# Performance work log

Hardware: AMD Instinct MI355X
Metric: run time of the kernel (lower is better)

## Reference

```python
import jax, jax.numpy as jnp
import numpy as np

B, L, D, E, N, DDELTA, DCONV = 4, 2048, 1024, 2048, 16, 64, 4
EPS = 1e-5


def setup_inputs() -> dict:
    key = jax.random.key(0)
    ks = jax.random.split(key, 12)
    def rn(k, shape, scale=0.02):
        return (jax.random.normal(k, shape) * scale).astype(jnp.float32)
    return {
        "resid":  jax.random.normal(ks[0], (B, L, D), dtype=jnp.float32),
        "norm_w": jnp.ones((D,), jnp.float32),
        "skip_w": rn(ks[1], (E, D)),          # skip_proj.weight
        "in_w":   rn(ks[2], (E, D)),          # in_proj.weight
        "conv_w": rn(ks[3], (E, 1, DCONV), 0.1),  # depthwise conv1d weight
        "conv_b": jnp.zeros((E,), jnp.float32),
        "Wd1":    rn(ks[4], (DDELTA, E)),     # W_delta_1.weight
        "Wd2_w":  rn(ks[5], (E, DDELTA)),     # W_delta_2.weight
        "Wd2_b":  rn(ks[6], (E,), 0.01),      # W_delta_2.bias
        "WB":     rn(ks[7], (N, E)),          # W_B.weight
        "WC":     rn(ks[8], (N, E)),          # W_C.weight
        "A_log":  (jax.random.normal(ks[9], (E, N)) * 0.5).astype(jnp.float32),
        "W_D":    jnp.ones((E,), jnp.float32),
        "out_w":  rn(ks[10], (D, E)),         # out_proj.weight
    }


def reference(resid, norm_w, skip_w, in_w, conv_w, conv_b, Wd1, Wd2_w, Wd2_b,
              WB, WC, A_log, W_D, out_w):
    # RMSNorm
    x = resid * jax.lax.rsqrt(jnp.mean(resid * resid, axis=-1, keepdims=True) + EPS) * norm_w
    skip = x @ skip_w.T                              # [B,L,E]
    x = x @ in_w.T                                   # [B,L,E]
    # depthwise causal conv1d (padding=DCONV-1 then truncate to L == left-pad only)
    xc = jnp.transpose(x, (0, 2, 1))                 # [B,E,L]
    xc = jax.lax.conv_general_dilated(
        xc, conv_w, window_strides=(1,), padding=[(DCONV - 1, 0)],
        dimension_numbers=("NCH", "OIH", "NCH"), feature_group_count=conv_w.shape[0])
    x = jnp.transpose(xc, (0, 2, 1)) + conv_b        # [B,L,E]
    x = jax.nn.silu(x)                               # ssm input

    A = -jnp.exp(A_log)                              # [E,N]
    delta = jax.nn.softplus((x @ Wd1.T) @ Wd2_w.T + Wd2_b)  # [B,L,E]
    Bm = x @ WB.T                                    # [B,L,N]
    Cm = x @ WC.T                                    # [B,L,N]

    def step(h, inp):
        x_l, d_l, B_l, C_l = inp                     # [B,E],[B,E],[B,N],[B,N]
        A_bar = jnp.exp(d_l[:, :, None] * A)         # [B,E,N]
        h = A_bar * h + (d_l * x_l)[:, :, None] * B_l[:, None, :]
        y_l = jnp.einsum("ben,bn->be", h, C_l)       # h @ C
        return h, y_l

    h0 = jnp.zeros((resid.shape[0], A.shape[0], A.shape[1]), x.dtype)
    xs = (jnp.swapaxes(x, 0, 1), jnp.swapaxes(delta, 0, 1),
          jnp.swapaxes(Bm, 0, 1), jnp.swapaxes(Cm, 0, 1))
    _, ys = jax.lax.scan(step, h0, xs)               # ys: [L,B,E]
    y = jnp.swapaxes(ys, 0, 1)                       # [B,L,E]

    y = y + x * W_D
    y = y * jax.nn.silu(skip)
    y = y @ out_w.T                                  # [B,L,D]
    return resid + y
```

## Files before the change

### kernel.cpp

```cpp
#include <hip/hip_runtime.h>
#include <hip/hip_bf16.h>
#include <math.h>

#define B_ 4
#define L_ 2048
#define D_ 1024
#define E_ 2048
#define N_ 16
#define DD_ 64
#define DCONV_ 4

#define S_SEG 32
#define SEGLEN_ (L_ / S_SEG)

typedef __attribute__((ext_vector_type(8))) short bf16x8;
typedef __attribute__((ext_vector_type(4))) float f32x4;

typedef __attribute__((address_space(1))) const void gvoid_t;
typedef __attribute__((address_space(3))) void lvoid_t;

static __device__ __forceinline__ float silu_f(float x) {
    return x / (1.f + __expf(-x));
}

static __device__ __forceinline__ ushort f2bf(float f) {
    __hip_bfloat16 h = __float2bfloat16(f);
    return *reinterpret_cast<ushort*>(&h);
}

static __device__ __forceinline__ float bf2f(ushort u) {
    uint v = ((uint)u) << 16;
    return __uint_as_float(v);
}

#define LOG2E_ 1.4426950408889634f

__global__ __launch_bounds__(256) void k_rmsnorm_bf(const float* __restrict__ resid,
                                                    const float* __restrict__ nw,
                                                    ushort* __restrict__ out) {
    int row = blockIdx.x;
    const float* r = resid + (size_t)row * D_;
    int t = threadIdx.x;
    float4 v = *reinterpret_cast<const float4*>(&r[t * 4]);
    float ss = v.x * v.x + v.y * v.y + v.z * v.z + v.w * v.w;
#pragma unroll
    for (int o = 32; o >= 1; o >>= 1) ss += __shfl_xor(ss, o, 64);
    __shared__ float red[4];
    if ((t & 63) == 0) red[t >> 6] = ss;
    __syncthreads();
    float tot = red[0] + red[1] + red[2] + red[3];
    float rs = rsqrtf(tot * (1.f / (float)D_) + 1e-5f);
    float4 w4 = *reinterpret_cast<const float4*>(&nw[t * 4]);
    ushort4 o4;
    o4.x = f2bf(v.x * rs * w4.x);
    o4.y = f2bf(v.y * rs * w4.y);
    o4.z = f2bf(v.z * rs * w4.z);
    o4.w = f2bf(v.w * rs * w4.w);
    *reinterpret_cast<ushort4*>(&out[(size_t)row * D_ + t * 4]) = o4;
}

__global__ __launch_bounds__(256) void k_cast_all(const float* __restrict__ skip_w,
                                                  const float* __restrict__ in_w,
                                                  const float* __restrict__ out_w,
                                                  const float* __restrict__ WB,
                                                  const float* __restrict__ WC,
                                                  const float* __restrict__ Wd1,
                                                  const float* __restrict__ Wd2,
                                                  ushort* __restrict__ w2,
                                                  ushort* __restrict__ outw,
                                                  ushort* __restrict__ wbc,
                                                  ushort* __restrict__ wd2) {
    int i = blockIdx.x * 256 + threadIdx.x;
    const float* src;
    ushort* dst;
    int off;
    if (i < 524288)       { src = skip_w; dst = w2;            off = i; }
    else if (i < 1048576) { src = in_w;   dst = w2 + 2097152;  off = i - 524288; }
    else if (i < 1572864) { src = out_w;  dst = outw;          off = i - 1048576; }
    else if (i < 1581056) { src = WB;     dst = wbc;           off = i - 1572864; }
    else if (i < 1589248) { src = WC;     dst = wbc + 32768;   off = i - 1581056; }
    else if (i < 1622016) { src = Wd1;    dst = wbc + 65536;   off = i - 1589248; }
    else                  { src = Wd2;    dst = wd2;           off = i - 1622016; }
    float4 v = *reinterpret_cast<const float4*>(&src[(size_t)off * 4]);
    ushort4 o;
    o.x = f2bf(v.x); o.y = f2bf(v.y); o.z = f2bf(v.z); o.w = f2bf(v.w);
    *reinterpret_cast<ushort4*>(&dst[(size_t)off * 4]) = o;
}

template <int EPI>
__global__ __launch_bounds__(256) void k_gemm_bf(const ushort* __restrict__ A,
                                                 const ushort* __restrict__ W,
                                                 const float* __restrict__ bias,
                                                 const float* __restrict__ addsrc,
                                                 float* __restrict__ Cf,
                                                 ushort* __restrict__ Cbf,
                                                 ushort* __restrict__ Cbf2,
                                                 int M, int N, int K) {
    constexpr int BM = 128, BN = 128, BK = 32;
    union SM {
        ushort stage[2 * BM * BK];
        float  epi[4][16][65];
    };
    __shared__ __align__(16) SM sm;
    ushort* As = sm.stage;
    ushort* Ws = sm.stage + BM * BK;

    int t = threadIdx.x;
    int m0 = blockIdx.y * BM, n0 = blockIdx.x * BN;
    int wave = t >> 6, lane = t & 63;
    int wr = wave >> 1, wc = wave & 1;
    int lr = lane & 15, lg = lane >> 4;
    int srow = lane >> 2;
    int scol = (lane & 3) * 8;

    f32x4 acc[4][4] = {};

    for (int k0 = 0; k0 < K; k0 += BK) {
#pragma unroll
        for (int p = 0; p < 2; ++p) {
            int seg = wave * 2 + p;
            int row = seg * 16 + srow;
            __builtin_amdgcn_global_load_lds(
                (gvoid_t*)(A + (size_t)(m0 + row) * K + k0 + scol),
                (lvoid_t*)(As + seg * 512), 16, 0, 0);
            __builtin_amdgcn_global_load_lds(
                (gvoid_t*)(W + (size_t)(n0 + row) * K + k0 + scol),
                (lvoid_t*)(Ws + seg * 512), 16, 0, 0);
        }
        __syncthreads();
        bf16x8 af[4], bfr[4];
#pragma unroll
        for (int i = 0; i < 4; ++i) {
            af[i]  = *reinterpret_cast<const bf16x8*>(&As[(wr * 64 + i * 16 + lr) * BK + lg * 8]);
            bfr[i] = *reinterpret_cast<const bf16x8*>(&Ws[(wc * 64 + i * 16 + lr) * BK + lg * 8]);
        }
#pragma unroll
        for (int i = 0; i < 4; ++i)
#pragma unroll
            for (int j = 0; j < 4; ++j)
                acc[i][j] = __builtin_amdgcn_mfma_f32_16x16x32_bf16(af[i], bfr[j], acc[i][j], 0, 0, 0);
        __syncthreads();
    }

    int er = lane >> 2;
    int ec = (lane & 3) * 16;
#pragma unroll
    for (int i = 0; i < 4; ++i) {
#pragma unroll
        for (int j = 0; j < 4; ++j)
#pragma unroll
            for (int q = 0; q < 4; ++q)
                sm.epi[wave][lg * 4 + q][j * 16 + lr] = acc[i][j][q];
        float vals[16];
#pragma unroll
        for (int v4 = 0; v4 < 4; ++v4) {
            f32x4 tmp = *reinterpret_cast<const f32x4*>(&sm.epi[wave][er][ec + v4 * 4]);
            vals[v4 * 4 + 0] = tmp[0]; vals[v4 * 4 + 1] = tmp[1];
            vals[v4 * 4 + 2] = tmp[2]; vals[v4 * 4 + 3] = tmp[3];
        }
        int grow = m0 + wr * 64 + i * 16 + er;
        int gcol = n0 + wc * 64 + ec;

        if (EPI == 1) {
            ushort u[16];
#pragma unroll
            for (int k = 0; k < 16; ++k) {
                float z = vals[k] + bias[gcol + k];
                u[k] = f2bf((z > 20.f) ? z : log1pf(expf(z)));
            }
            *reinterpret_cast<uint4*>(&Cbf[(size_t)grow * N + gcol]) = *reinterpret_cast<uint4*>(&u[0]);
            *reinterpret_cast<uint4*>(&Cbf[(size_t)grow * N + gcol + 8]) = *reinterpret_cast<uint4*>(&u[8]);
        } else if (EPI == 2) {
#pragma unroll
            for (int v4 = 0; v4 < 4; ++v4) {
                f32x4 r4 = *reinterpret_cast<const f32x4*>(&addsrc[(size_t)grow * N + gcol + v4 * 4]);
                f32x4 o4;
#pragma unroll
                for (int k = 0; k < 4; ++k) o4[k] = vals[v4 * 4 + k] + r4[k];
                *reinterpret_cast<f32x4*>(&Cf[(size_t)grow * N + gcol + v4 * 4]) = o4;
            }
        } else {
            ushort u[16];
#pragma unroll
            for (int k = 0; k < 16; ++k) u[k] = f2bf(vals[k]);
            if (gcol < 2048) {
                *reinterpret_cast<uint4*>(&Cbf[(size_t)grow * 2048 + gcol]) = *reinterpret_cast<uint4*>(&u[0]);
                *reinterpret_cast<uint4*>(&Cbf[(size_t)grow * 2048 + gcol + 8]) = *reinterpret_cast<uint4*>(&u[8]);
            } else {
                int c2 = gcol - 2048;
                *reinterpret_cast<uint4*>(&Cbf2[(size_t)grow * 2048 + c2]) = *reinterpret_cast<uint4*>(&u[0]);
                *reinterpret_cast<uint4*>(&Cbf2[(size_t)grow * 2048 + c2 + 8]) = *reinterpret_cast<uint4*>(&u[8]);
            }
        }
    }
}

__global__ __launch_bounds__(256) void k_proj(const ushort* __restrict__ A,
                                              const ushort* __restrict__ Wc,
                                              float* __restrict__ Bm,
                                              float* __restrict__ Cm,
                                              ushort* __restrict__ d1_bf) {
    constexpr int BK = 32, LDB = 40;
    __shared__ __align__(16) ushort As[32 * LDB];
    __shared__ __align__(16) ushort Ws[96 * LDB];
    int t = threadIdx.x;
    int m0 = blockIdx.x * 32;
    int wave = t >> 6, lane = t & 63;
    int rowbase = (wave >> 1) * 16;
    int colbase = (wave & 1) * 48;
    int lr = lane & 15, lg = lane >> 4;

    f32x4 acc[3] = {};

    for (int k0 = 0; k0 < E_; k0 += BK) {
        if (t < 128) {
            int row = t >> 2;
            int cg = (t & 3) * 8;
            *reinterpret_cast<uint4*>(&As[row * LDB + cg]) =
                *reinterpret_cast<const uint4*>(&A[(size_t)(m0 + row) * E_ + k0 + cg]);
        }
        {
            int row = t >> 2, cg = (t & 3) * 8;
            *reinterpret_cast<uint4*>(&Ws[row * LDB + cg]) =
                *reinterpret_cast<const uint4*>(&Wc[(size_t)row * E_ + k0 + cg]);
            if (t < 128) {
                int f2 = t + 256;
                int row2 = f2 >> 2, cg2 = (f2 & 3) * 8;
                *reinterpret_cast<uint4*>(&Ws[row2 * LDB + cg2]) =
                    *reinterpret_cast<const uint4*>(&Wc[(size_t)row2 * E_ + k0 + cg2]);
            }
        }
        __syncthreads();
        bf16x8 af = *reinterpret_cast<const bf16x8*>(&As[(rowbase + lr) * LDB + lg * 8]);
#pragma unroll
        for (int j = 0; j < 3; ++j) {
            bf16x8 bf = *reinterpret_cast<const bf16x8*>(&Ws[(colbase + j * 16 + lr) * LDB + lg * 8]);
            acc[j] = __builtin_amdgcn_mfma_f32_16x16x32_bf16(af, bf, acc[j], 0, 0, 0);
        }
        __syncthreads();
    }

#pragma unroll
    for (int j = 0; j < 3; ++j) {
        int ncol = colbase + j * 16 + lr;
#pragma unroll
        for (int q = 0; q < 4; ++q) {
            int m = m0 + rowbase + lg * 4 + q;
            float v = acc[j][q];
            if (ncol < 16)      Bm[(size_t)m * 16 + ncol] = v;
            else if (ncol < 32) Cm[(size_t)m * 16 + (ncol - 16)] = v;
            else                d1_bf[(size_t)m * 64 + (ncol - 32)] = f2bf(v);
        }
    }
}

__global__ __launch_bounds__(256) void k_conv_silu(const ushort* __restrict__ x,
                                                   const float* __restrict__ w,
                                                   const float* __restrict__ bias,
                                                   ushort* __restrict__ out_bf) {
    int idx = blockIdx.x * 256 + threadIdx.x;
    int e = idx & (E_ - 1);
    int l = (idx / E_) & (L_ - 1);
    float4 wv = *reinterpret_cast<const float4*>(&w[e * 4]);
    float acc = bias[e];
    acc = fmaf(wv.w, bf2f(x[idx]), acc);
    if (l >= 1) acc = fmaf(wv.z, bf2f(x[idx - E_]), acc);
    if (l >= 2) acc = fmaf(wv.y, bf2f(x[idx - 2 * E_]), acc);
    if (l >= 3) acc = fmaf(wv.x, bf2f(x[idx - 3 * E_]), acc);
    out_bf[idx] = f2bf(silu_f(acc));
}

__global__ __launch_bounds__(256, 4) void k_scan_p1(const ushort* __restrict__ xs,
                                                    const ushort* __restrict__ delta,
                                                    const float* __restrict__ Bm,
                                                    const float* __restrict__ A_log,
                                                    float* __restrict__ hbuf,
                                                    float* __restrict__ sdsum) {
    int t = threadIdx.x;
    int bid = blockIdx.x;
    int s = bid & (S_SEG - 1);
    int eblk = (bid >> 5) & 7;
    int b = bid >> 8;
    int e = eblk * 256 + t;

    float A2[16];
#pragma unroll
    for (int i = 0; i < 16; i += 4) {
        f32x4 al = *reinterpret_cast<const f32x4*>(&A_log[(size_t)e * 16 + i]);
#pragma unroll
        for (int j = 0; j < 4; ++j) A2[i + j] = -__expf(al[j]) * LOG2E_;
    }
    f32x4 h4[4] = {};
    float sdl = 0.f;

    const ushort* dp = delta + ((size_t)b * L_ + s * SEGLEN_) * E_ + e;
    const ushort* xp = xs    + ((size_t)b * L_ + s * SEGLEN_) * E_ + e;
    const float*  Bp = Bm + ((size_t)b * L_ + s * SEGLEN_) * 16;

    auto compute = [&](ushort du, ushort xu, int l) {
        float d = bf2f(du), xv = bf2f(xu);
        float dx = d * xv;
        sdl += d;
#pragma unroll
        for (int g = 0; g < 4; ++g) {
            f32x4 Bv = *reinterpret_cast<const f32x4*>(&Bp[l * 16 + g * 4]);
            f32x4 e4;
#pragma unroll
            for (int j = 0; j < 4; ++j) e4[j] = exp2f(d * A2[g * 4 + j]);
            h4[g] = e4 * h4[g] + dx * Bv;
        }
    };

    ushort duA = dp[0], xuA = xp[0];
    for (int l = 0; l < SEGLEN_; l += 2) {
        ushort duB = dp[(l + 1) * E_], xuB = xp[(l + 1) * E_];
        compute(duA, xuA, l);
        int ln = l + 2; if (ln > SEGLEN_ - 1) ln = SEGLEN_ - 1;
        duA = dp[ln * E_]; xuA = xp[ln * E_];
        compute(duB, xuB, l + 1);
    }

    size_t cidx = ((size_t)(b * S_SEG + s) * E_ + e) * 16;
#pragma unroll
    for (int g = 0; g < 4; ++g)
        *reinterpret_cast<f32x4*>(&hbuf[cidx + g * 4]) = h4[g];
    sdsum[(size_t)(b * S_SEG + s) * E_ + e] = sdl;
}

__global__ __launch_bounds__(256) void k_scan_p2(float* __restrict__ hbuf,
                                                 const float* __restrict__ sdsum,
                                                 const float* __restrict__ A_log) {
    int t = blockIdx.x * 256 + threadIdx.x;
    int q = t & 3;
    int e = (t >> 2) & (E_ - 1);
    int b = t >> 13;
    f32x4 A2;
    {
        f32x4 al = *reinterpret_cast<const f32x4*>(&A_log[(size_t)e * 16 + q * 4]);
#pragma unroll
        for (int i = 0; i < 4; ++i) A2[i] = -__expf(al[i]) * LOG2E_;
    }
    f32x4 acc = {0.f, 0.f, 0.f, 0.f};
    for (int s = 0; s < S_SEG; ++s) {
        size_t idx = ((size_t)(b * S_SEG + s) * E_ + e) * 16 + q * 4;
        f32x4 hl = *reinterpret_cast<const f32x4*>(&hbuf[idx]);
        float sd = sdsum[(size_t)(b * S_SEG + s) * E_ + e];
        *reinterpret_cast<f32x4*>(&hbuf[idx]) = acc;
        f32x4 p;
#pragma unroll
        for (int i = 0; i < 4; ++i) p[i] = exp2f(A2[i] * sd);
        acc = hl + p * acc;
    }
}

__global__ __launch_bounds__(256, 4) void k_scan_p3(const ushort* __restrict__ xs,
                                                    const ushort* __restrict__ delta,
                                                    const float* __restrict__ Bm,
                                                    const float* __restrict__ Cm,
                                                    const float* __restrict__ A_log,
                                                    const float* __restrict__ W_D,
                                                    const ushort* __restrict__ skip,
                                                    const float* __restrict__ hbuf,
                                                    ushort* __restrict__ yg) {
    int t = threadIdx.x;
    int bid = blockIdx.x;
    int s = bid & (S_SEG - 1);
    int eblk = (bid >> 5) & 7;
    int b = bid >> 8;
    int e = eblk * 256 + t;

    float A2[16];
#pragma unroll
    for (int i = 0; i < 16; i += 4) {
        f32x4 al = *reinterpret_cast<const f32x4*>(&A_log[(size_t)e * 16 + i]);
#pragma unroll
        for (int j = 0; j < 4; ++j) A2[i + j] = -__expf(al[j]) * LOG2E_;
    }
    size_t cidx = ((size_t)(b * S_SEG + s) * E_ + e) * 16;
    f32x4 h4[4];
#pragma unroll
    for (int g = 0; g < 4; ++g)
        h4[g] = *reinterpret_cast<const f32x4*>(&hbuf[cidx + g * 4]);
    float wd = W_D[e];

    const ushort* dp = delta + ((size_t)b * L_ + s * SEGLEN_) * E_ + e;
    const ushort* xp = xs    + ((size_t)b * L_ + s * SEGLEN_) * E_ + e;
    const ushort* sp = skip  + ((size_t)b * L_ + s * SEGLEN_) * E_ + e;
    const float*  Bp = Bm + ((size_t)b * L_ + s * SEGLEN_) * 16;
    const float*  Cp = Cm + ((size_t)b * L_ + s * SEGLEN_) * 16;
    ushort* yp = yg + ((size_t)b * L_ + s * SEGLEN_) * E_ + e;

    auto compute = [&](ushort du, ushort xu, ushort su, int l) {
        float d = bf2f(du), xv = bf2f(xu);
        float dx = d * xv;
        f32x4 yv = {0.f, 0.f, 0.f, 0.f};
#pragma unroll
        for (int g = 0; g < 4; ++g) {
            f32x4 Bv = *reinterpret_cast<const f32x4*>(&Bp[l * 16 + g * 4]);
            f32x4 Cv = *reinterpret_cast<const f32x4*>(&Cp[l * 16 + g * 4]);
            f32x4 e4;
#pragma unroll
            for (int j = 0; j < 4; ++j) e4[j] = exp2f(d * A2[g * 4 + j]);
            h4[g] = e4 * h4[g] + dx * Bv;
            yv = h4[g] * Cv + yv;
        }
        float y = (yv[0] + yv[1]) + (yv[2] + yv[3]);
        float gsk = silu_f(bf2f(su));
        yp[(size_t)l * E_] = f2bf((y + xv * wd) * gsk);
    };

    ushort duA = dp[0], xuA = xp[0], suA = sp[0];
    for (int l = 0; l < SEGLEN_; l += 2) {
        ushort duB = dp[(l + 1) * E_], xuB = xp[(l + 1) * E_], suB = sp[(l + 1) * E_];
        compute(duA, xuA, suA, l);
        int ln = l + 2; if (ln > SEGLEN_ - 1) ln = SEGLEN_ - 1;
        duA = dp[ln * E_]; xuA = xp[ln * E_]; suA = sp[ln * E_];
        compute(duB, xuB, suB, l + 1);
    }
}

extern "C" void kernel_launch(void* const* d_in, const int* in_sizes, int n_in,
                              void* d_out, int out_size, void* d_ws, size_t ws_size,
                              hipStream_t stream) {
    const float* resid  = (const float*)d_in[0];
    const float* norm_w = (const float*)d_in[1];
    const float* skip_w = (const float*)d_in[2];
    const float* in_w   = (const float*)d_in[3];
    const float* conv_w = (const float*)d_in[4];
    const float* conv_b = (const float*)d_in[5];
    const float* Wd1    = (const float*)d_in[6];
    const float* Wd2_w  = (const float*)d_in[7];
    const float* Wd2_b  = (const float*)d_in[8];
    const float* WB     = (const float*)d_in[9];
    const float* WC     = (const float*)d_in[10];
    const float* A_log  = (const float*)d_in[11];
    const float* W_D    = (const float*)d_in[12];
    const float* out_w  = (const float*)d_in[13];
    float* out = (float*)d_out;

    const int M = B_ * L_;
    char* p = (char*)d_ws;
    ushort* xn_bf    = (ushort*)p; p += (size_t)M * D_ * 2;
    ushort* w2_bf    = (ushort*)p; p += (size_t)2 * E_ * D_ * 2;
    ushort* outw_bf  = (ushort*)p; p += (size_t)D_ * E_ * 2;
    ushort* wbc_bf   = (ushort*)p; p += (size_t)96 * E_ * 2;
    ushort* wd2_bf   = (ushort*)p; p += (size_t)E_ * DD_ * 2;
    ushort* xin_bf   = (ushort*)p; p += (size_t)M * E_ * 2;
    ushort* xs_bf    = (ushort*)p; p += (size_t)M * E_ * 2;
    ushort* skip_bf  = (ushort*)p; p += (size_t)M * E_ * 2;
    ushort* delta_bf = (ushort*)p; p += (size_t)M * E_ * 2;
    ushort* yg_bf    = (ushort*)p; p += (size_t)M * E_ * 2;
    ushort* d1_bf    = (ushort*)p; p += (size_t)M * DD_ * 2;
    float*  Bm       = (float*)p;  p += (size_t)M * 16 * 4;
    float*  Cm       = (float*)p;  p += (size_t)M * 16 * 4;
    float*  hbuf     = (float*)xn_bf;
    float*  sdsum    = (float*)w2_bf;

    dim3 blk(256);

    k_cast_all<<<dim3(6464), blk, 0, stream>>>(skip_w, in_w, out_w, WB, WC, Wd1, Wd2_w,
                                               w2_bf, outw_bf, wbc_bf, wd2_bf);
    k_rmsnorm_bf<<<dim3(M), blk, 0, stream>>>(resid, norm_w, xn_bf);
    k_gemm_bf<3><<<dim3(2 * E_ / 128, M / 128), blk, 0, stream>>>(
        xn_bf, w2_bf, nullptr, nullptr, nullptr, skip_bf, xin_bf, M, 2 * E_, D_);
    k_conv_silu<<<dim3((M * E_) / 256), blk, 0, stream>>>(xin_bf, conv_w, conv_b, xs_bf);
    k_proj<<<dim3(M / 32), blk, 0, stream>>>(xs_bf, wbc_bf, Bm, Cm, d1_bf);
    k_gemm_bf<1><<<dim3(E_ / 128, M / 128), blk, 0, stream>>>(
        d1_bf, wd2_bf, Wd2_b, nullptr, nullptr, delta_bf, nullptr, M, E_, DD_);
    k_scan_p1<<<dim3(B_ * S_SEG * (E_ / 256)), blk, 0, stream>>>(xs_bf, delta_bf, Bm, A_log, hbuf, sdsum);
    k_scan_p2<<<dim3((B_ * E_ * 4) / 256), blk, 0, stream>>>(hbuf, sdsum, A_log);
    k_scan_p3<<<dim3(B_ * S_SEG * (E_ / 256)), blk, 0, stream>>>(xs_bf, delta_bf, Bm, Cm, A_log,
                                                                  W_D, skip_bf, hbuf, yg_bf);
    k_gemm_bf<2><<<dim3(D_ / 128, M / 128), blk, 0, stream>>>(
        yg_bf, outw_bf, nullptr, resid, out, nullptr, nullptr, M, D_, E_);
}
```

Measured before the change: 623.9 us.

## Split-K the B/C/delta projection, double scan segments, pad epilogue LDS

The narrow projection GEMM (K=2048, N=96) is split four ways along K, with partial sums written to scratch and reduced by a new kernel. Its grid was only 256 blocks, so this aims to fill the GPU, at the cost of extra global traffic and one more launch. The chunked scan now uses 64 segments per sequence with a higher occupancy hint, which gives more parallel blocks but more carry state. The GEMM epilogue LDS row pitch changes from 65 to 68. hbuf and sdsum now get dedicated workspace, and the aliased buffer is reused for the projection partials.

New measurement: 658.9 us. +5.6%, slower.

```diff
diff --git a/kernel.cpp b/kernel.cpp
--- a/kernel.cpp
+++ b/kernel.cpp
@@ -10,8 +10,11 @@
 #define DD_ 64
 #define DCONV_ 4
 
-#define S_SEG 32
+#define S_SEG 64
 #define SEGLEN_ (L_ / S_SEG)
+
+#define KS_ 4
+#define KSUB_ (E_ / KS_)
 
 typedef __attribute__((ext_vector_type(8))) short bf16x8;
 typedef __attribute__((ext_vector_type(4))) float f32x4;
@@ -97,9 +100,10 @@
                                                  ushort* __restrict__ Cbf2,
                                                  int M, int N, int K) {
     constexpr int BM = 128, BN = 128, BK = 32;
+    constexpr int EPAD = 68;
     union SM {
         ushort stage[2 * BM * BK];
-        float  epi[4][16][65];
+        float  epi[4][16][EPAD];
     };
     __shared__ __align__(16) SM sm;
     ushort* As = sm.stage;
@@ -197,14 +201,13 @@
 
 __global__ __launch_bounds__(256) void k_proj(const ushort* __restrict__ A,
                                               const ushort* __restrict__ Wc,
-                                              float* __restrict__ Bm,
-                                              float* __restrict__ Cm,
-                                              ushort* __restrict__ d1_bf) {
+                                              float* __restrict__ part) {
     constexpr int BK = 32, LDB = 40;
     __shared__ __align__(16) ushort As[32 * LDB];
     __shared__ __align__(16) ushort Ws[96 * LDB];
     int t = threadIdx.x;
     int m0 = blockIdx.x * 32;
+    int ks = blockIdx.y;
     int wave = t >> 6, lane = t & 63;
     int rowbase = (wave >> 1) * 16;
     int colbase = (wave & 1) * 48;
@@ -212,7 +215,7 @@
 
     f32x4 acc[3] = {};
 
-    for (int k0 = 0; k0 < E_; k0 += BK) {
+    for (int k0 = ks * KSUB_; k0 < (ks + 1) * KSUB_; k0 += BK) {
         if (t < 128) {
             int row = t >> 2;
             int cg = (t & 3) * 8;
@@ -246,12 +249,24 @@
 #pragma unroll
         for (int q = 0; q < 4; ++q) {
             int m = m0 + rowbase + lg * 4 + q;
-            float v = acc[j][q];
-            if (ncol < 16)      Bm[(size_t)m * 16 + ncol] = v;
-            else if (ncol < 32) Cm[(size_t)m * 16 + (ncol - 16)] = v;
-            else                d1_bf[(size_t)m * 64 + (ncol - 32)] = f2bf(v);
-        }
-    }
+            part[((size_t)ks * (B_ * L_) + m) * 96 + ncol] = acc[j][q];
+        }
+    }
+}
+
+__global__ __launch_bounds__(256) void k_proj_sum(const float* __restrict__ part,
+                                                  float* __restrict__ Bm,
+                                                  float* __restrict__ Cm,
+                                                  ushort* __restrict__ d1_bf) {
+    int idx = blockIdx.x * 256 + threadIdx.x;
+    int m = idx / 96, c = idx - m * 96;
+    float v = 0.f;
+#pragma unroll
+    for (int ks = 0; ks < KS_; ++ks)
+        v += part[((size_t)ks * (B_ * L_) + m) * 96 + c];
+    if (c < 16)      Bm[(size_t)m * 16 + c] = v;
+    else if (c < 32) Cm[(size_t)m * 16 + (c - 16)] = v;
+    else             d1_bf[(size_t)m * 64 + (c - 32)] = f2bf(v);
 }
 
 __global__ __launch_bounds__(256) void k_conv_silu(const ushort* __restrict__ x,
@@ -270,7 +285,7 @@
     out_bf[idx] = f2bf(silu_f(acc));
 }
 
-__global__ __launch_bounds__(256, 4) void k_scan_p1(const ushort* __restrict__ xs,
+__global__ __launch_bounds__(256, 8) void k_scan_p1(const ushort* __restrict__ xs,
                                                     const ushort* __restrict__ delta,
                                                     const float* __restrict__ Bm,
                                                     const float* __restrict__ A_log,
@@ -279,8 +294,8 @@
     int t = threadIdx.x;
     int bid = blockIdx.x;
     int s = bid & (S_SEG - 1);
-    int eblk = (bid >> 5) & 7;
-    int b = bid >> 8;
+    int eblk = (bid >> 6) & 7;
+    int b = bid >> 9;
     int e = eblk * 256 + t;
 
     float A2[16];
@@ -353,7 +368,7 @@
     }
 }
 
-__global__ __launch_bounds__(256, 4) void k_scan_p3(const ushort* __restrict__ xs,
+__global__ __launch_bounds__(256, 8) void k_scan_p3(const ushort* __restrict__ xs,
                                                     const ushort* __restrict__ delta,
                                                     const float* __restrict__ Bm,
                                                     const float* __restrict__ Cm,
@@ -365,8 +380,8 @@
     int t = threadIdx.x;
     int bid = blockIdx.x;
     int s = bid & (S_SEG - 1);
-    int eblk = (bid >> 5) & 7;
-    int b = bid >> 8;
+    int eblk = (bid >> 6) & 7;
+    int b = bid >> 9;
     int e = eblk * 256 + t;
 
     float A2[16];
@@ -453,8 +468,9 @@
     ushort* d1_bf    = (ushort*)p; p += (size_t)M * DD_ * 2;
     float*  Bm       = (float*)p;  p += (size_t)M * 16 * 4;
     float*  Cm       = (float*)p;  p += (size_t)M * 16 * 4;
-    float*  hbuf     = (float*)xn_bf;
-    float*  sdsum    = (float*)w2_bf;
+    float*  hbuf     = (float*)p;  p += (size_t)B_ * S_SEG * E_ * 16 * 4;
+    float*  sdsum    = (float*)p;  p += (size_t)B_ * S_SEG * E_ * 4;
+    float*  proj_part = (float*)xn_bf;
 
     dim3 blk(256);
 
@@ -464,7 +480,8 @@
     k_gemm_bf<3><<<dim3(2 * E_ / 128, M / 128), blk, 0, stream>>>(
         xn_bf, w2_bf, nullptr, nullptr, nullptr, skip_bf, xin_bf, M, 2 * E_, D_);
     k_conv_silu<<<dim3((M * E_) / 256), blk, 0, stream>>>(xin_bf, conv_w, conv_b, xs_bf);
-    k_proj<<<dim3(M / 32), blk, 0, stream>>>(xs_bf, wbc_bf, Bm, Cm, d1_bf);
+    k_proj<<<dim3(M / 32, KS_), blk, 0, stream>>>(xs_bf, wbc_bf, proj_part);
+    k_proj_sum<<<dim3((M * 96) / 256), blk, 0, stream>>>(proj_part, Bm, Cm, d1_bf);
     k_gemm_bf<1><<<dim3(E_ / 128, M / 128), blk, 0, stream>>>(
         d1_bf, wd2_bf, Wd2_b, nullptr, nullptr, delta_bf, nullptr, M, E_, DD_);
     k_scan_p1<<<dim3(B_ * S_SEG * (E_ / 256)), blk, 0, stream>>>(xs_bf, delta_bf, Bm, A_log, hbuf, sdsum);
```
